# Performance work log

Hardware: AMD Instinct MI355X
Metric: run time of the kernel (lower is better)

## Reference

```python
import jax, jax.numpy as jnp
import numpy as np

N = 16384      # nodes
E = 131072     # edges
D = 768        # in_size = hid_size = out_size (LayerNorm(768) hardcoded)
NT = 4         # num edge types (TypedLinear num_types)
NB = 3         # num bases (basis regularizer)
LN_EPS = 1e-5


def _layernorm(x, gamma, beta):
    mu = jnp.mean(x, axis=-1, keepdims=True)
    var = jnp.mean(jnp.square(x - mu), axis=-1, keepdims=True)
    return (x - mu) * jax.lax.rsqrt(var + LN_EPS) * gamma + beta


def setup_inputs() -> dict:
    key = jax.random.key(0)
    ks = jax.random.split(key, 16)
    s = 0.02  # weight init scale
    return {
        "h": jax.random.normal(ks[0], (N, D), jnp.float32),
        # TypedLinear basis params: W = sum_b coeff[t,b] * basis[b]
        "W_text": jax.random.normal(ks[1], (NB, D, D), jnp.float32) * s,
        "coeff_text": jax.random.normal(ks[2], (NT, NB), jnp.float32),
        "W_user": jax.random.normal(ks[3], (NB, D, D), jnp.float32) * s,
        "coeff_user": jax.random.normal(ks[4], (NT, NB), jnp.float32),
        "W_dst": jax.random.normal(ks[5], (NB, D, D), jnp.float32) * s,
        "coeff_dst": jax.random.normal(ks[6], (NT, NB), jnp.float32),
        "ln_gamma": jnp.ones((D,), jnp.float32),
        "ln_beta": jnp.zeros((D,), jnp.float32),
        "W_lin": jax.random.normal(ks[7], (2 * D, D), jnp.float32) * s,
        "b_lin": jnp.zeros((D,), jnp.float32),
        "src": jax.random.randint(ks[8], (E,), 0, N, dtype=jnp.int32),
        "dst": jax.random.randint(ks[9], (E,), 0, N, dtype=jnp.int32),
        "etype": jax.random.randint(ks[10], (E,), 0, NT, dtype=jnp.int32),
        "hete": jax.random.randint(ks[11], (E,), 0, 2, dtype=jnp.int32),
    }


def reference(h, W_text, coeff_text, W_user, coeff_user, W_dst, coeff_dst,
              ln_gamma, ln_beta, W_lin, b_lin, src, dst, etype, hete):
    # eval mode: dropout = identity
    x = _layernorm(h, ln_gamma, ln_beta)                       # [N, D]
    # Typed-linear via basis decomposition, folded per (type, node): [NT, N, D]
    Ht = jnp.einsum('nd,bdh,tb->tnh', x, W_text, coeff_text)
    Hu = jnp.einsum('nd,bdh,tb->tnh', x, W_user, coeff_user)
    Hd = jnp.einsum('nd,bdh,tb->tnh', x, W_dst, coeff_dst)

    mask = hete > 0                                            # hete vs homo edges
    # per-edge routed source message: [E, D]
    ef = jnp.where(mask[:, None],
                   jax.nn.relu(Ht[etype, src]),
                   jax.nn.relu(Hu[etype, src]))
    # Original concatenates [hete_feat, homo_feat] along edge dim, i.e. a stable
    # permutation putting hete edges first; dst features stay in original order.
    perm = jnp.argsort((~mask).astype(jnp.int32), stable=True)
    feat_perm = ef[perm]                                       # [E, D]
    dfeat = jax.nn.relu(Hd[etype, dst])                        # [E, D]
    m = jnp.concatenate([feat_perm, dfeat], axis=-1)           # [E, 2D]
    # scatter-sum messages to destination nodes
    n = jax.ops.segment_sum(m, dst, num_segments=N)            # [N, 2D]
    z = jax.nn.relu(n @ W_lin + b_lin)                         # [N, D]
    zn = jnp.linalg.norm(z, ord=2, axis=1, keepdims=True)
    zn = jnp.where(zn == 0, jnp.asarray(1.0, z.dtype), zn)
    return z / zn
```

## Files before the change

### kernel.cpp

```cpp
#include <hip/hip_runtime.h>
#include <hip/hip_bf16.h>
#include <cstdint>

static constexpr int N_  = 16384;
static constexpr int E_  = 131072;
static constexpr int D_  = 768;
static constexpr int D2_ = 1536;
static constexpr int DSQ_ = D_ * D_;

static constexpr size_t OFF_XB   = 0;
static constexpr size_t OFF_WBT  = 25165824;
static constexpr size_t OFF_WLT  = 39321600;
static constexpr size_t OFF_NB16 = 41680896;
static constexpr size_t OFF_Y3   = 92012544;
static constexpr size_t OFF_ZB   = 92012544;
static constexpr size_t OFF_N1C  = 192675840;
static constexpr size_t OFF_PAY  = 217841664;
static constexpr size_t OFF_CNT  = 218365952;
static constexpr size_t OFF_CURH = 218628096;
static constexpr size_t OFF_CURU = 218693632;
static constexpr size_t OFF_BASE = 218759168;
static constexpr size_t OFF_BC   = 218824736;
static constexpr size_t OFF_SCAN = 218826784;

typedef __attribute__((ext_vector_type(8))) short short8v;
typedef __attribute__((ext_vector_type(4))) float floatx4;

__device__ __forceinline__ void gld16(const void* g, void* l) {
  __builtin_amdgcn_global_load_lds(
      (const __attribute__((address_space(1))) unsigned int*)g,
      (__attribute__((address_space(3))) unsigned int*)l, 16, 0, 0);
}

__device__ __forceinline__ float b2f(short u) {
  union { unsigned int i; float f; } x;
  x.i = ((unsigned int)(unsigned short)u) << 16;
  return x.f;
}

__device__ __forceinline__ float wave_sum(float v) {
#pragma unroll
  for (int o = 32; o; o >>= 1) v += __shfl_down(v, o, 64);
  return v;
}

__global__ __launch_bounds__(256) void wbasis_t_kernel(
    const float* __restrict__ Wt, const float* __restrict__ Wu,
    const float* __restrict__ Wd, __hip_bfloat16* __restrict__ WbT) {
  __shared__ float tile[64][65];
  int fb = blockIdx.y;
  int f = fb / 3, b = fb % 3;
  const float* W = ((f == 0) ? Wt : ((f == 1) ? Wu : Wd)) + (size_t)b * DSQ_;
  int dt = (blockIdx.x / 12) * 64;
  int ht = (blockIdx.x % 12) * 64;
  int tid = threadIdx.x;
#pragma unroll
  for (int jj = 0; jj < 16; jj++) {
    int idx = jj * 256 + tid;
    int rr = idx >> 6, cc = idx & 63;
    tile[rr][cc] = W[(size_t)(dt + rr) * D_ + ht + cc];
  }
  __syncthreads();
#pragma unroll
  for (int jj = 0; jj < 16; jj++) {
    int idx = jj * 256 + tid;
    int hh = idx >> 6, dd = idx & 63;
    WbT[(size_t)fb * DSQ_ + (size_t)(ht + hh) * D_ + dt + dd] =
        __float2bfloat16(tile[dd][hh]);
  }
}

__global__ __launch_bounds__(256) void wlint_kernel(
    const float* __restrict__ W, __hip_bfloat16* __restrict__ WT) {
  int i = blockIdx.x * 256 + threadIdx.x;
  int k = i / D_, h = i % D_;
  WT[(size_t)h * D2_ + k] = __float2bfloat16(W[i]);
}

__global__ __launch_bounds__(256) void ln_kernel(
    const float* __restrict__ h, const float* __restrict__ gamma,
    const float* __restrict__ beta, __hip_bfloat16* __restrict__ x) {
  int v = blockIdx.x, tid = threadIdx.x;
  const float* hr = h + (size_t)v * D_;
  float e0 = hr[tid], e1 = hr[tid + 256], e2 = hr[tid + 512];
  float s = e0 + e1 + e2;
  float q = e0 * e0 + e1 * e1 + e2 * e2;
  __shared__ float red[8];
  __shared__ float mv[2];
  float ws_ = wave_sum(s), wq = wave_sum(q);
  int lane = tid & 63, w = tid >> 6;
  if (lane == 0) { red[w] = ws_; red[4 + w] = wq; }
  __syncthreads();
  if (tid == 0) {
    float S = red[0] + red[1] + red[2] + red[3];
    float Q = red[4] + red[5] + red[6] + red[7];
    float mu = S * (1.0f / D_);
    float var = Q * (1.0f / D_) - mu * mu;
    mv[0] = mu;
    mv[1] = rsqrtf(var + 1e-5f);
  }
  __syncthreads();
  float mu = mv[0], rstd = mv[1];
  __hip_bfloat16* xr = x + (size_t)v * D_;
  xr[tid]       = __float2bfloat16((e0 - mu) * rstd * gamma[tid]       + beta[tid]);
  xr[tid + 256] = __float2bfloat16((e1 - mu) * rstd * gamma[tid + 256] + beta[tid + 256]);
  xr[tid + 512] = __float2bfloat16((e2 - mu) * rstd * gamma[tid + 512] + beta[tid + 512]);
}

__global__ __launch_bounds__(256) void edge_a_kernel(
    const int* __restrict__ hete, const int* __restrict__ dst,
    const int* __restrict__ etype, int* __restrict__ blockcnt,
    int* __restrict__ cnt4) {
  int j = blockIdx.x * 256 + threadIdx.x;
  int flag = hete[j] > 0;
  unsigned long long m = __ballot(flag);
  __shared__ int wsum[4];
  int lane = threadIdx.x & 63, w = threadIdx.x >> 6;
  if (lane == 0) wsum[w] = __popcll(m);
  __syncthreads();
  if (threadIdx.x == 0)
    blockcnt[blockIdx.x] = wsum[0] + wsum[1] + wsum[2] + wsum[3];
  atomicAdd(&cnt4[dst[j] * 4 + etype[j]], 1);
}

__global__ __launch_bounds__(1024) void fused_scan_kernel(
    const int* __restrict__ blockcnt, int* __restrict__ scanout,
    const int* __restrict__ cnt4, int* __restrict__ base) {
  int t = threadIdx.x;
  if (blockIdx.x == 0) {
    __shared__ int s[1024];
    int v = (t < 512) ? blockcnt[t] : 0;
    s[t] = v;
    __syncthreads();
    for (int o = 1; o < 512; o <<= 1) {
      int add = (t >= o) ? s[t - o] : 0;
      __syncthreads();
      s[t] += add;
      __syncthreads();
    }
    if (t < 512) scanout[t] = s[t] - v;
    if (t == 511) scanout[512] = s[511];
  } else {
    __shared__ int s[1024];
    int loc[16];
    int sum = 0;
#pragma unroll
    for (int i = 0; i < 16; i++) {
      int v = t * 16 + i;
      int d = cnt4[v * 4] + cnt4[v * 4 + 1] + cnt4[v * 4 + 2] + cnt4[v * 4 + 3];
      loc[i] = sum;
      sum += d;
    }
    s[t] = sum;
    __syncthreads();
    for (int o = 1; o < 1024; o <<= 1) {
      int add = (t >= o) ? s[t - o] : 0;
      __syncthreads();
      s[t] += add;
      __syncthreads();
    }
    int pre = t ? s[t - 1] : 0;
#pragma unroll
    for (int i = 0; i < 16; i++) base[t * 16 + i] = pre + loc[i];
    if (t == 1023) base[N_] = s[1023];
  }
}

__global__ __launch_bounds__(256) void edge_bsort_kernel(
    const int* __restrict__ hete, const int* __restrict__ dst,
    const int* __restrict__ src, const int* __restrict__ etype,
    const int* __restrict__ scanout, const int* __restrict__ base,
    int* __restrict__ curH, int* __restrict__ curU,
    int* __restrict__ payload) {
  int j = blockIdx.x * 256 + threadIdx.x;
  int flag = hete[j] > 0;
  unsigned long long m = __ballot(flag);
  __shared__ int wsum[4];
  int lane = threadIdx.x & 63, w = threadIdx.x >> 6;
  if (lane == 0) wsum[w] = __popcll(m);
  __syncthreads();
  int wpre = 0;
#pragma unroll
  for (int i = 0; i < 4; i++) wpre += (i < w) ? wsum[i] : 0;
  int lpre = __popcll(m & ((1ull << lane) - 1ull));
  int hcum = scanout[blockIdx.x] + wpre + lpre;
  int K = scanout[512];
  int e = flag ? hcum : (K + j - hcum);
  int v = dst[e];
  int p;
  if (flag) p = base[v] + atomicAdd(&curH[v], 1);
  else      p = base[v + 1] - 1 - atomicAdd(&curU[v], 1);
  payload[p] = (etype[j] << 14) | src[j];
}

template <bool FIRST, int SEG>
__global__ __launch_bounds__(256) void gather_n1_kernel(
    const __hip_bfloat16* __restrict__ Y, const float* __restrict__ coeff,
    const int* __restrict__ base, const int* __restrict__ hcnt,
    const int* __restrict__ payload, __hip_bfloat16* __restrict__ n1c,
    __hip_bfloat16* __restrict__ nb16) {
  int wv = threadIdx.x >> 6, lane = threadIdx.x & 63;
  int v = blockIdx.x * 4 + wv;
  int bh = base[v] + hcnt[v];
  int lo = (SEG == 0) ? base[v] : bh;
  int hi = (SEG == 0) ? bh : base[v + 1];
  float cf[12];
#pragma unroll
  for (int i = 0; i < 12; i++) cf[i] = coeff[i];
  float acc[12];
  if (FIRST) {
#pragma unroll
    for (int i = 0; i < 12; i++) acc[i] = 0.f;
  } else {
    short8v a8 = *(const short8v*)(n1c + (size_t)v * D_ + lane * 8);
    short4  b4 = *(const short4*)(n1c + (size_t)v * D_ + 512 + lane * 4);
#pragma unroll
    for (int i = 0; i < 8; i++) acc[i] = b2f(a8[i]);
    acc[8] = b2f(b4.x); acc[9] = b2f(b4.y);
    acc[10] = b2f(b4.z); acc[11] = b2f(b4.w);
  }
  const size_t YS = (size_t)N_ * D_;
  for (int idx = lo; idx < hi; ++idx) {
    int pl = payload[idx];
    int t = pl >> 14;
    float c0 = cf[t * 3], c1 = cf[t * 3 + 1], c2 = cf[t * 3 + 2];
    const __hip_bfloat16* r0 = Y + (size_t)(pl & 16383) * D_;
    short8v a0 = *(const short8v*)(r0 + lane * 8);
    short8v a1 = *(const short8v*)(r0 + YS + lane * 8);
    short8v a2 = *(const short8v*)(r0 + 2 * YS + lane * 8);
    short4  b0v = *(const short4*)(r0 + 512 + lane * 4);
    short4  b1v = *(const short4*)(r0 + YS + 512 + lane * 4);
    short4  b2v = *(const short4*)(r0 + 2 * YS + 512 + lane * 4);
#pragma unroll
    for (int i = 0; i < 8; i++)
      acc[i] += fmaxf(c0 * b2f(a0[i]) + c1 * b2f(a1[i]) + c2 * b2f(a2[i]), 0.f);
    acc[8]  += fmaxf(c0 * b2f(b0v.x) + c1 * b2f(b1v.x) + c2 * b2f(b2v.x), 0.f);
    acc[9]  += fmaxf(c0 * b2f(b0v.y) + c1 * b2f(b1v.y) + c2 * b2f(b2v.y), 0.f);
    acc[10] += fmaxf(c0 * b2f(b0v.z) + c1 * b2f(b1v.z) + c2 * b2f(b2v.z), 0.f);
    acc[11] += fmaxf(c0 * b2f(b0v.w) + c1 * b2f(b1v.w) + c2 * b2f(b2v.w), 0.f);
  }
  __hip_bfloat16 o[12];
#pragma unroll
  for (int i = 0; i < 12; i++) o[i] = __float2bfloat16(acc[i]);
  if (FIRST) {
    *(short8v*)(n1c + (size_t)v * D_ + lane * 8) = *(const short8v*)o;
    *(short4*)(n1c + (size_t)v * D_ + 512 + lane * 4) = *(const short4*)(o + 8);
  } else {
    *(short8v*)(nb16 + (size_t)v * D2_ + lane * 8) = *(const short8v*)o;
    *(short4*)(nb16 + (size_t)v * D2_ + 512 + lane * 4) = *(const short4*)(o + 8);
  }
}

__global__ __launch_bounds__(256) void combine_n2_kernel(
    const __hip_bfloat16* __restrict__ Y, const float* __restrict__ cd,
    const int* __restrict__ cnt4, __hip_bfloat16* __restrict__ nb16) {
  size_t i = ((size_t)blockIdx.x * 256 + threadIdx.x) * 8;
  int v = (int)(i / D_);
  int k = (int)(i % D_);
  const size_t YS = (size_t)N_ * D_;
  short8v y0 = *(const short8v*)(Y + i);
  short8v y1 = *(const short8v*)(Y + YS + i);
  short8v y2 = *(const short8v*)(Y + 2 * YS + i);
  float f0[8], f1[8], f2[8];
#pragma unroll
  for (int j = 0; j < 8; j++) {
    f0[j] = b2f(y0[j]); f1[j] = b2f(y1[j]); f2[j] = b2f(y2[j]);
  }
  float acc[8] = {0.f, 0.f, 0.f, 0.f, 0.f, 0.f, 0.f, 0.f};
#pragma unroll
  for (int t = 0; t < 4; t++) {
    float c = (float)cnt4[v * 4 + t];
    if (c != 0.f) {
      float d0 = cd[t * 3], d1 = cd[t * 3 + 1], d2 = cd[t * 3 + 2];
#pragma unroll
      for (int j = 0; j < 8; j++)
        acc[j] += c * fmaxf(d0 * f0[j] + d1 * f1[j] + d2 * f2[j], 0.f);
    }
  }
  __hip_bfloat16 o[8];
#pragma unroll
  for (int j = 0; j < 8; j++) o[j] = __float2bfloat16(acc[j]);
  *(short8v*)(nb16 + (size_t)v * D2_ + D_ + k) = *(const short8v*)o;
}

template <bool BIAS, bool RELU>
__global__ __launch_bounds__(256) void gemm_mfma_kernel(
    const __hip_bfloat16* __restrict__ A, const __hip_bfloat16* __restrict__ BT0,
    const float* __restrict__ bias, __hip_bfloat16* __restrict__ C0,
    int M, int N, int K, size_t strideB, size_t strideC) {
  __shared__ char lds[32768];
  char* As = lds;
  char* Bs = lds + 16384;
  int tid = threadIdx.x;
  int lane = tid & 63;
  int wv = tid >> 6;
  int wr = wv >> 1, wc = wv & 1;
  int gx = gridDim.x, gz = gridDim.z;
  int nwg = gx * gridDim.y * gz;
  int id = (blockIdx.z * gridDim.y + blockIdx.y) * gx + blockIdx.x;
  int s = (id & 7) * (nwg >> 3) + (id >> 3);
  int bx = s % gx;
  int rem = s / gx;
  int z = rem % gz;
  int by = rem / gz;
  const __hip_bfloat16* BT = BT0 + (size_t)z * strideB;
  int row0 = by * 128, col0 = bx * 128;
  int r_ = tid >> 3;
  int s_ = tid & 7;

  floatx4 acc[4][4];
#pragma unroll
  for (int i = 0; i < 4; i++)
#pragma unroll
    for (int j = 0; j < 4; j++) acc[i][j] = floatx4{0.f, 0.f, 0.f, 0.f};

  for (int k0 = 0; k0 < K; k0 += 64) {
    __syncthreads();
#pragma unroll
    for (int is = 0; is < 4; is++) {
      int r = is * 32 + r_;
      int sp = s_ ^ (r & 7);
      gld16(A  + (size_t)(row0 + r) * K + k0 + sp * 8, As + is * 4096 + tid * 16);
      gld16(BT + (size_t)(col0 + r) * K + k0 + sp * 8, Bs + is * 4096 + tid * 16);
    }
    __syncthreads();
#pragma unroll
    for (int kk = 0; kk < 64; kk += 32) {
      int p = (kk >> 3) + (lane >> 4);
      short8v af[4], bf[4];
#pragma unroll
      for (int m = 0; m < 4; m++) {
        int ra = wr * 64 + m * 16 + (lane & 15);
        af[m] = *(const short8v*)(As + ra * 128 + ((p ^ (ra & 7)) << 4));
        int rb = wc * 64 + m * 16 + (lane & 15);
        bf[m] = *(const short8v*)(Bs + rb * 128 + ((p ^ (rb & 7)) << 4));
      }
#pragma unroll
      for (int m = 0; m < 4; m++)
#pragma unroll
        for (int n = 0; n < 4; n++)
          acc[m][n] = __builtin_amdgcn_mfma_f32_16x16x32_bf16(
              af[m], bf[n], acc[m][n], 0, 0, 0);
    }
  }
  __syncthreads();
  char* cs = lds + wv * 8192;
#pragma unroll
  for (int m = 0; m < 4; m++) {
#pragma unroll
    for (int n = 0; n < 4; n++) {
      int c = n * 16 + (lane & 15);
      float bv = BIAS ? bias[col0 + wc * 64 + c] : 0.f;
#pragma unroll
      for (int q = 0; q < 4; q++) {
        int r = m * 16 + (lane >> 4) * 4 + q;
        float v = acc[m][n][q] + bv;
        if (RELU) v = fmaxf(v, 0.f);
        int byte = r * 128 + ((((c >> 3) + r) & 7) << 4) + ((c & 7) << 1);
        *(__hip_bfloat16*)(cs + byte) = __float2bfloat16(v);
      }
    }
  }
  __hip_bfloat16* C = C0 + (size_t)z * strideC;
#pragma unroll
  for (int i = 0; i < 8; i++) {
    int r = i * 8 + (lane >> 3);
    int s8 = lane & 7;
    int p = (s8 + r) & 7;
    short8v v = *(const short8v*)(cs + r * 128 + (p << 4));
    int grow = row0 + wr * 64 + r;
    int gcol = col0 + wc * 64 + s8 * 8;
    *(short8v*)(C + (size_t)grow * N + gcol) = v;
  }
}

__global__ __launch_bounds__(256) void norm_kernel(
    const __hip_bfloat16* __restrict__ z, float* __restrict__ out) {
  int v = blockIdx.x, tid = threadIdx.x;
  float e[4] = {0.f, 0.f, 0.f, 0.f};
  if (tid < 192) {
    short4 a = *(const short4*)(z + (size_t)v * D_ + tid * 4);
    e[0] = b2f(a.x); e[1] = b2f(a.y); e[2] = b2f(a.z); e[3] = b2f(a.w);
  }
  float q = e[0] * e[0] + e[1] * e[1] + e[2] * e[2] + e[3] * e[3];
  __shared__ float red[4];
  __shared__ float sc;
  float wq = wave_sum(q);
  int lane = tid & 63, w = tid >> 6;
  if (lane == 0) red[w] = wq;
  __syncthreads();
  if (tid == 0) {
    float S = red[0] + red[1] + red[2] + red[3];
    float norm = sqrtf(S);
    sc = (norm == 0.f) ? 1.f : (1.f / norm);
  }
  __syncthreads();
  if (tid < 192) {
    float s = sc;
    float4 o = {e[0] * s, e[1] * s, e[2] * s, e[3] * s};
    *(float4*)(out + (size_t)v * D_ + tid * 4) = o;
  }
}

extern "C" void kernel_launch(void* const* d_in, const int* in_sizes, int n_in,
                              void* d_out, int out_size, void* d_ws,
                              size_t ws_size, hipStream_t stream) {
  (void)in_sizes; (void)n_in; (void)out_size; (void)ws_size;
  const float* h      = (const float*)d_in[0];
  const float* W_text = (const float*)d_in[1];
  const float* c_text = (const float*)d_in[2];
  const float* W_user = (const float*)d_in[3];
  const float* c_user = (const float*)d_in[4];
  const float* W_dst  = (const float*)d_in[5];
  const float* c_dst  = (const float*)d_in[6];
  const float* gamma  = (const float*)d_in[7];
  const float* beta   = (const float*)d_in[8];
  const float* W_lin  = (const float*)d_in[9];
  const float* b_lin  = (const float*)d_in[10];
  const int* src      = (const int*)d_in[11];
  const int* dst      = (const int*)d_in[12];
  const int* etype    = (const int*)d_in[13];
  const int* hete     = (const int*)d_in[14];
  float* out          = (float*)d_out;

  char* ws = (char*)d_ws;
  __hip_bfloat16* xb   = (__hip_bfloat16*)(ws + OFF_XB);
  __hip_bfloat16* WbT  = (__hip_bfloat16*)(ws + OFF_WBT);
  __hip_bfloat16* WlT  = (__hip_bfloat16*)(ws + OFF_WLT);
  __hip_bfloat16* nb16 = (__hip_bfloat16*)(ws + OFF_NB16);
  __hip_bfloat16* Y3   = (__hip_bfloat16*)(ws + OFF_Y3);
  __hip_bfloat16* zbuf = (__hip_bfloat16*)(ws + OFF_ZB);
  __hip_bfloat16* n1c  = (__hip_bfloat16*)(ws + OFF_N1C);
  int* payload  = (int*)(ws + OFF_PAY);
  int* cnt4     = (int*)(ws + OFF_CNT);
  int* curH     = (int*)(ws + OFF_CURH);
  int* curU     = (int*)(ws + OFF_CURU);
  int* base     = (int*)(ws + OFF_BASE);
  int* blockcnt = (int*)(ws + OFF_BC);
  int* scanout  = (int*)(ws + OFF_SCAN);

  hipMemsetAsync(cnt4, 0, 262144 + 65536 + 65536, stream);

  wbasis_t_kernel<<<dim3(144, 9), 256, 0, stream>>>(W_text, W_user, W_dst, WbT);
  wlint_kernel<<<(D2_ * D_) / 256, 256, 0, stream>>>(W_lin, WlT);
  ln_kernel<<<N_, 256, 0, stream>>>(h, gamma, beta, xb);
  edge_a_kernel<<<E_ / 256, 256, 0, stream>>>(hete, dst, etype, blockcnt, cnt4);
  fused_scan_kernel<<<2, 1024, 0, stream>>>(blockcnt, scanout, cnt4, base);
  edge_bsort_kernel<<<E_ / 256, 256, 0, stream>>>(hete, dst, src, etype,
                                                  scanout, base, curH, curU,
                                                  payload);

  const size_t HSTRIDE = (size_t)N_ * D_;
  const dim3 ggrid(D_ / 128, N_ / 128, 3);

  gemm_mfma_kernel<false, false><<<ggrid, 256, 0, stream>>>(
      xb, WbT + (size_t)6 * DSQ_, nullptr, Y3, N_, D_, D_, DSQ_, HSTRIDE);
  combine_n2_kernel<<<(N_ * D_) / (256 * 8), 256, 0, stream>>>(Y3, c_dst,
                                                               cnt4, nb16);
  gemm_mfma_kernel<false, false><<<ggrid, 256, 0, stream>>>(
      xb, WbT, nullptr, Y3, N_, D_, D_, DSQ_, HSTRIDE);
  gather_n1_kernel<true, 0><<<N_ / 4, 256, 0, stream>>>(
      Y3, c_text, base, curH, payload, n1c, nb16);
  gemm_mfma_kernel<false, false><<<ggrid, 256, 0, stream>>>(
      xb, WbT + (size_t)3 * DSQ_, nullptr, Y3, N_, D_, D_, DSQ_, HSTRIDE);
  gather_n1_kernel<false, 1><<<N_ / 4, 256, 0, stream>>>(
      Y3, c_user, base, curH, payload, n1c, nb16);

  gemm_mfma_kernel<true, true><<<dim3(D_ / 128, N_ / 128, 1), 256, 0, stream>>>(
      nb16, WlT, b_lin, zbuf, N_, D_, D2_, 0, 0);
  norm_kernel<<<N_, 256, 0, stream>>>(zbuf, out);
}
```

Baseline: 470.3 us.

## Merge text/user GEMMs and gathers into one pass when workspace allows

When the workspace is large enough, the text and user basis GEMMs run as a single 6-slice launch into one big Y buffer. A single merged gather kernel then reads both halves per destination node, instead of two gathers that round-trip an n1c intermediate. The weight transpose kernels are merged into one tiled launch, and the layernorm kernel is vectorized with float4 loads. This trades a larger workspace footprint for fewer launches and less intermediate traffic, and falls back to the old path when the workspace is small.

```diff
diff --git a/kernel.cpp b/kernel.cpp
--- a/kernel.cpp
+++ b/kernel.cpp
@@ -8,20 +8,34 @@
 static constexpr int D2_ = 1536;
 static constexpr int DSQ_ = D_ * D_;
 
-static constexpr size_t OFF_XB   = 0;
-static constexpr size_t OFF_WBT  = 25165824;
-static constexpr size_t OFF_WLT  = 39321600;
-static constexpr size_t OFF_NB16 = 41680896;
-static constexpr size_t OFF_Y3   = 92012544;
-static constexpr size_t OFF_ZB   = 92012544;
-static constexpr size_t OFF_N1C  = 192675840;
-static constexpr size_t OFF_PAY  = 217841664;
-static constexpr size_t OFF_CNT  = 218365952;
-static constexpr size_t OFF_CURH = 218628096;
-static constexpr size_t OFF_CURU = 218693632;
-static constexpr size_t OFF_BASE = 218759168;
-static constexpr size_t OFF_BC   = 218824736;
-static constexpr size_t OFF_SCAN = 218826784;
+static constexpr size_t S_XB   = 0;
+static constexpr size_t S_WBT  = 25165824;
+static constexpr size_t S_WLT  = 39321600;
+static constexpr size_t S_NB16 = 41680896;
+static constexpr size_t S_Y3   = 92012544;
+static constexpr size_t S_ZB   = 92012544;
+static constexpr size_t S_N1C  = 192675840;
+static constexpr size_t S_PAY  = 217841664;
+static constexpr size_t S_CNT  = 218365952;
+static constexpr size_t S_CURH = 218628096;
+static constexpr size_t S_CURU = 218693632;
+static constexpr size_t S_BASE = 218759168;
+static constexpr size_t S_BC   = 218824736;
+static constexpr size_t S_SCAN = 218826784;
+
+static constexpr size_t B_XB   = 0;
+static constexpr size_t B_WBT  = 25165824;
+static constexpr size_t B_WLT  = 35782656;
+static constexpr size_t B_NB16 = 38141952;
+static constexpr size_t B_PAY  = 88473600;
+static constexpr size_t B_CNT  = 88997888;
+static constexpr size_t B_CURH = 89260032;
+static constexpr size_t B_CURU = 89325568;
+static constexpr size_t B_BASE = 89391104;
+static constexpr size_t B_BC   = 89456672;
+static constexpr size_t B_SCAN = 89458720;
+static constexpr size_t B_YBIG = 89460992;
+static constexpr size_t B_NEED = 240455936;
 
 typedef __attribute__((ext_vector_type(8))) short short8v;
 typedef __attribute__((ext_vector_type(4))) float floatx4;
@@ -44,47 +58,68 @@
   return v;
 }
 
-__global__ __launch_bounds__(256) void wbasis_t_kernel(
+__global__ __launch_bounds__(256) void wprep_kernel(
     const float* __restrict__ Wt, const float* __restrict__ Wu,
-    const float* __restrict__ Wd, __hip_bfloat16* __restrict__ WbT) {
+    const float* __restrict__ Wd, const float* __restrict__ Wl,
+    __hip_bfloat16* __restrict__ WbT, __hip_bfloat16* __restrict__ WlT) {
   __shared__ float tile[64][65];
-  int fb = blockIdx.y;
-  int f = fb / 3, b = fb % 3;
-  const float* W = ((f == 0) ? Wt : ((f == 1) ? Wu : Wd)) + (size_t)b * DSQ_;
-  int dt = (blockIdx.x / 12) * 64;
-  int ht = (blockIdx.x % 12) * 64;
+  int y = blockIdx.y;
   int tid = threadIdx.x;
-#pragma unroll
-  for (int jj = 0; jj < 16; jj++) {
-    int idx = jj * 256 + tid;
-    int rr = idx >> 6, cc = idx & 63;
-    tile[rr][cc] = W[(size_t)(dt + rr) * D_ + ht + cc];
-  }
-  __syncthreads();
-#pragma unroll
-  for (int jj = 0; jj < 16; jj++) {
-    int idx = jj * 256 + tid;
-    int hh = idx >> 6, dd = idx & 63;
-    WbT[(size_t)fb * DSQ_ + (size_t)(ht + hh) * D_ + dt + dd] =
-        __float2bfloat16(tile[dd][hh]);
-  }
-}
-
-__global__ __launch_bounds__(256) void wlint_kernel(
-    const float* __restrict__ W, __hip_bfloat16* __restrict__ WT) {
-  int i = blockIdx.x * 256 + threadIdx.x;
-  int k = i / D_, h = i % D_;
-  WT[(size_t)h * D2_ + k] = __float2bfloat16(W[i]);
+  if (y < 9) {
+    int f = y / 3, b = y % 3;
+    const float* W = ((f == 0) ? Wt : ((f == 1) ? Wu : Wd)) + (size_t)b * DSQ_;
+    int dt = (blockIdx.x / 12) * 64;
+    int ht = (blockIdx.x % 12) * 64;
+#pragma unroll
+    for (int jj = 0; jj < 16; jj++) {
+      int idx = jj * 256 + tid;
+      int rr = idx >> 6, cc = idx & 63;
+      tile[rr][cc] = W[(size_t)(dt + rr) * D_ + ht + cc];
+    }
+    __syncthreads();
+#pragma unroll
+    for (int jj = 0; jj < 16; jj++) {
+      int idx = jj * 256 + tid;
+      int hh = idx >> 6, dd = idx & 63;
+      WbT[(size_t)y * DSQ_ + (size_t)(ht + hh) * D_ + dt + dd] =
+          __float2bfloat16(tile[dd][hh]);
+    }
+  } else {
+    int idx0 = (y - 9) * 144 + blockIdx.x;
+    int kt = (idx0 % 24) * 64;
+    int ht = (idx0 / 24) * 64;
+#pragma unroll
+    for (int jj = 0; jj < 16; jj++) {
+      int idx = jj * 256 + tid;
+      int rr = idx >> 6, cc = idx & 63;
+      tile[rr][cc] = Wl[(size_t)(kt + rr) * D_ + ht + cc];
+    }
+    __syncthreads();
+#pragma unroll
+    for (int jj = 0; jj < 16; jj++) {
+      int idx = jj * 256 + tid;
+      int hh = idx >> 6, dd = idx & 63;
+      WlT[(size_t)(ht + hh) * D2_ + kt + dd] = __float2bfloat16(tile[dd][hh]);
+    }
+  }
 }
 
 __global__ __launch_bounds__(256) void ln_kernel(
     const float* __restrict__ h, const float* __restrict__ gamma,
     const float* __restrict__ beta, __hip_bfloat16* __restrict__ x) {
   int v = blockIdx.x, tid = threadIdx.x;
-  const float* hr = h + (size_t)v * D_;
-  float e0 = hr[tid], e1 = hr[tid + 256], e2 = hr[tid + 512];
-  float s = e0 + e1 + e2;
-  float q = e0 * e0 + e1 * e1 + e2 * e2;
+  float e[4] = {0.f, 0.f, 0.f, 0.f};
+  float g[4], bta[4];
+  if (tid < 192) {
+    float4 a = *(const float4*)(h + (size_t)v * D_ + tid * 4);
+    e[0] = a.x; e[1] = a.y; e[2] = a.z; e[3] = a.w;
+    float4 gg = *(const float4*)(gamma + tid * 4);
+    float4 bb = *(const float4*)(beta + tid * 4);
+    g[0] = gg.x; g[1] = gg.y; g[2] = gg.z; g[3] = gg.w;
+    bta[0] = bb.x; bta[1] = bb.y; bta[2] = bb.z; bta[3] = bb.w;
+  }
+  float s = e[0] + e[1] + e[2] + e[3];
+  float q = e[0] * e[0] + e[1] * e[1] + e[2] * e[2] + e[3] * e[3];
   __shared__ float red[8];
   __shared__ float mv[2];
   float ws_ = wave_sum(s), wq = wave_sum(q);
@@ -100,11 +135,14 @@
     mv[1] = rsqrtf(var + 1e-5f);
   }
   __syncthreads();
-  float mu = mv[0], rstd = mv[1];
-  __hip_bfloat16* xr = x + (size_t)v * D_;
-  xr[tid]       = __float2bfloat16((e0 - mu) * rstd * gamma[tid]       + beta[tid]);
-  xr[tid + 256] = __float2bfloat16((e1 - mu) * rstd * gamma[tid + 256] + beta[tid + 256]);
-  xr[tid + 512] = __float2bfloat16((e2 - mu) * rstd * gamma[tid + 512] + beta[tid + 512]);
+  if (tid < 192) {
+    float mu = mv[0], rstd = mv[1];
+    __hip_bfloat16 o[4];
+#pragma unroll
+    for (int i = 0; i < 4; i++)
+      o[i] = __float2bfloat16((e[i] - mu) * rstd * g[i] + bta[i]);
+    *(short4*)(x + (size_t)v * D_ + tid * 4) = *(const short4*)o;
+  }
 }
 
 __global__ __launch_bounds__(256) void edge_a_kernel(
@@ -249,6 +287,52 @@
     *(short8v*)(nb16 + (size_t)v * D2_ + lane * 8) = *(const short8v*)o;
     *(short4*)(nb16 + (size_t)v * D2_ + 512 + lane * 4) = *(const short4*)(o + 8);
   }
+}
+
+__global__ __launch_bounds__(256) void gather_merged_kernel(
+    const __hip_bfloat16* __restrict__ Yt, const __hip_bfloat16* __restrict__ Yu,
+    const float* __restrict__ c_text, const float* __restrict__ c_user,
+    const int* __restrict__ base, const int* __restrict__ hcnt,
+    const int* __restrict__ payload, __hip_bfloat16* __restrict__ nb16) {
+  int wv = threadIdx.x >> 6, lane = threadIdx.x & 63;
+  int v = blockIdx.x * 4 + wv;
+  int lo = base[v];
+  int bh = lo + hcnt[v];
+  int hi = base[v + 1];
+  float cf[24];
+#pragma unroll
+  for (int i = 0; i < 12; i++) { cf[i] = c_text[i]; cf[12 + i] = c_user[i]; }
+  float acc[12];
+#pragma unroll
+  for (int i = 0; i < 12; i++) acc[i] = 0.f;
+  const size_t YS = (size_t)N_ * D_;
+  for (int idx = lo; idx < hi; ++idx) {
+    int pl = payload[idx];
+    bool isU = idx >= bh;
+    const __hip_bfloat16* Y = isU ? Yu : Yt;
+    int t = pl >> 14;
+    const float* c = cf + (isU ? 12 : 0) + t * 3;
+    float c0 = c[0], c1 = c[1], c2 = c[2];
+    const __hip_bfloat16* r0 = Y + (size_t)(pl & 16383) * D_;
+    short8v a0 = *(const short8v*)(r0 + lane * 8);
+    short8v a1 = *(const short8v*)(r0 + YS + lane * 8);
+    short8v a2 = *(const short8v*)(r0 + 2 * YS + lane * 8);
+    short4  b0v = *(const short4*)(r0 + 512 + lane * 4);
+    short4  b1v = *(const short4*)(r0 + YS + 512 + lane * 4);
+    short4  b2v = *(const short4*)(r0 + 2 * YS + 512 + lane * 4);
+#pragma unroll
+    for (int i = 0; i < 8; i++)
+      acc[i] += fmaxf(c0 * b2f(a0[i]) + c1 * b2f(a1[i]) + c2 * b2f(a2[i]), 0.f);
+    acc[8]  += fmaxf(c0 * b2f(b0v.x) + c1 * b2f(b1v.x) + c2 * b2f(b2v.x), 0.f);
+    acc[9]  += fmaxf(c0 * b2f(b0v.y) + c1 * b2f(b1v.y) + c2 * b2f(b2v.y), 0.f);
+    acc[10] += fmaxf(c0 * b2f(b0v.z) + c1 * b2f(b1v.z) + c2 * b2f(b2v.z), 0.f);
+    acc[11] += fmaxf(c0 * b2f(b0v.w) + c1 * b2f(b1v.w) + c2 * b2f(b2v.w), 0.f);
+  }
+  __hip_bfloat16 o[12];
+#pragma unroll
+  for (int i = 0; i < 12; i++) o[i] = __float2bfloat16(acc[i]);
+  *(short8v*)(nb16 + (size_t)v * D2_ + lane * 8) = *(const short8v*)o;
+  *(short4*)(nb16 + (size_t)v * D2_ + 512 + lane * 4) = *(const short4*)(o + 8);
 }
 
 __global__ __launch_bounds__(256) void combine_n2_kernel(
@@ -405,7 +489,7 @@
 extern "C" void kernel_launch(void* const* d_in, const int* in_sizes, int n_in,
                               void* d_out, int out_size, void* d_ws,
                               size_t ws_size, hipStream_t stream) {
-  (void)in_sizes; (void)n_in; (void)out_size; (void)ws_size;
+  (void)in_sizes; (void)n_in; (void)out_size;
   const float* h      = (const float*)d_in[0];
   const float* W_text = (const float*)d_in[1];
   const float* c_text = (const float*)d_in[2];
@@ -423,26 +507,25 @@
   const int* hete     = (const int*)d_in[14];
   float* out          = (float*)d_out;
 
+  const bool big = ws_size >= (size_t)B_NEED;
   char* ws = (char*)d_ws;
-  __hip_bfloat16* xb   = (__hip_bfloat16*)(ws + OFF_XB);
-  __hip_bfloat16* WbT  = (__hip_bfloat16*)(ws + OFF_WBT);
-  __hip_bfloat16* WlT  = (__hip_bfloat16*)(ws + OFF_WLT);
-  __hip_bfloat16* nb16 = (__hip_bfloat16*)(ws + OFF_NB16);
-  __hip_bfloat16* Y3   = (__hip_bfloat16*)(ws + OFF_Y3);
-  __hip_bfloat16* zbuf = (__hip_bfloat16*)(ws + OFF_ZB);
-  __hip_bfloat16* n1c  = (__hip_bfloat16*)(ws + OFF_N1C);
-  int* payload  = (int*)(ws + OFF_PAY);
-  int* cnt4     = (int*)(ws + OFF_CNT);
-  int* curH     = (int*)(ws + OFF_CURH);
-  int* curU     = (int*)(ws + OFF_CURU);
-  int* base     = (int*)(ws + OFF_BASE);
-  int* blockcnt = (int*)(ws + OFF_BC);
-  int* scanout  = (int*)(ws + OFF_SCAN);
+  const size_t HSTRIDE = (size_t)N_ * D_;
+
+  __hip_bfloat16* xb   = (__hip_bfloat16*)(ws + (big ? B_XB : S_XB));
+  __hip_bfloat16* WbT  = (__hip_bfloat16*)(ws + (big ? B_WBT : S_WBT));
+  __hip_bfloat16* WlT  = (__hip_bfloat16*)(ws + (big ? B_WLT : S_WLT));
+  __hip_bfloat16* nb16 = (__hip_bfloat16*)(ws + (big ? B_NB16 : S_NB16));
+  int* payload  = (int*)(ws + (big ? B_PAY : S_PAY));
+  int* cnt4     = (int*)(ws + (big ? B_CNT : S_CNT));
+  int* curH     = (int*)(ws + (big ? B_CURH : S_CURH));
+  int* curU     = (int*)(ws + (big ? B_CURU : S_CURU));
+  int* base     = (int*)(ws + (big ? B_BASE : S_BASE));
+  int* blockcnt = (int*)(ws + (big ? B_BC : S_BC));
+  int* scanout  = (int*)(ws + (big ? B_SCAN : S_SCAN));
 
   hipMemsetAsync(cnt4, 0, 262144 + 65536 + 65536, stream);
-
-  wbasis_t_kernel<<<dim3(144, 9), 256, 0, stream>>>(W_text, W_user, W_dst, WbT);
-  wlint_kernel<<<(D2_ * D_) / 256, 256, 0, stream>>>(W_lin, WlT);
+  wprep_kernel<<<dim3(144, 11), 256, 0, stream>>>(W_text, W_user, W_dst,
+                                                  W_lin, WbT, WlT);
   ln_kernel<<<N_, 256, 0, stream>>>(h, gamma, beta, xb);
   edge_a_kernel<<<E_ / 256, 256, 0, stream>>>(hete, dst, etype, blockcnt, cnt4);
   fused_scan_kernel<<<2, 1024, 0, stream>>>(blockcnt, scanout, cnt4, base);
@@ -450,23 +533,48 @@
                                                   scanout, base, curH, curU,
                                                   payload);
 
-  const size_t HSTRIDE = (size_t)N_ * D_;
-  const dim3 ggrid(D_ / 128, N_ / 128, 3);
-
-  gemm_mfma_kernel<false, false><<<ggrid, 256, 0, stream>>>(
-      xb, WbT + (size_t)6 * DSQ_, nullptr, Y3, N_, D_, D_, DSQ_, HSTRIDE);
-  combine_n2_kernel<<<(N_ * D_) / (256 * 8), 256, 0, stream>>>(Y3, c_dst,
-                                                               cnt4, nb16);
-  gemm_mfma_kernel<false, false><<<ggrid, 256, 0, stream>>>(
-      xb, WbT, nullptr, Y3, N_, D_, D_, DSQ_, HSTRIDE);
-  gather_n1_kernel<true, 0><<<N_ / 4, 256, 0, stream>>>(
-      Y3, c_text, base, curH, payload, n1c, nb16);
-  gemm_mfma_kernel<false, false><<<ggrid, 256, 0, stream>>>(
-      xb, WbT + (size_t)3 * DSQ_, nullptr, Y3, N_, D_, D_, DSQ_, HSTRIDE);
-  gather_n1_kernel<false, 1><<<N_ / 4, 256, 0, stream>>>(
-      Y3, c_user, base, curH, payload, n1c, nb16);
-
-  gemm_mfma_kernel<true, true><<<dim3(D_ / 128, N_ / 128, 1), 256, 0, stream>>>(
-      nb16, WlT, b_lin, zbuf, N_, D_, D2_, 0, 0);
-  norm_kernel<<<N_, 256, 0, stream>>>(zbuf, out);
-}
+  if (big) {
+    __hip_bfloat16* Ybig = (__hip_bfloat16*)(ws + B_YBIG);
+    __hip_bfloat16* zbuf = Ybig;
+    gemm_mfma_kernel<false, false>
+        <<<dim3(D_ / 128, N_ / 128, 3), 256, 0, stream>>>(
+            xb, WbT + (size_t)6 * DSQ_, nullptr, Ybig, N_, D_, D_, DSQ_,
+            HSTRIDE);
+    combine_n2_kernel<<<(N_ * D_) / (256 * 8), 256, 0, stream>>>(Ybig, c_dst,
+                                                                 cnt4, nb16);
+    gemm_mfma_kernel<false, false>
+        <<<dim3(D_ / 128, N_ / 128, 6), 256, 0, stream>>>(
+            xb, WbT, nullptr, Ybig, N_, D_, D_, DSQ_, HSTRIDE);
+    gather_merged_kernel<<<N_ / 4, 256, 0, stream>>>(
+        Ybig, Ybig + 3 * HSTRIDE, c_text, c_user, base, curH, payload, nb16);
+    gemm_mfma_kernel<true, true>
+        <<<dim3(D_ / 128, N_ / 128, 1), 256, 0, stream>>>(
+            nb16, WlT, b_lin, zbuf, N_, D_, D2_, 0, 0);
+    norm_kernel<<<N_, 256, 0, stream>>>(zbuf, out);
+  } else {
+    __hip_bfloat16* Y3   = (__hip_bfloat16*)(ws + S_Y3);
+    __hip_bfloat16* zbuf = (__hip_bfloat16*)(ws + S_ZB);
+    __hip_bfloat16* n1c  = (__hip_bfloat16*)(ws + S_N1C);
+    gemm_mfma_kernel<false, false>
+        <<<dim3(D_ / 128, N_ / 128, 3), 256, 0, stream>>>(
+            xb, WbT + (size_t)6 * DSQ_, nullptr, Y3, N_, D_, D_, DSQ_,
+            HSTRIDE);
+    combine_n2_kernel<<<(N_ * D_) / (256 * 8), 256, 0, stream>>>(Y3, c_dst,
+                                                                 cnt4, nb16);
+    gemm_mfma_kernel<false, false>
+        <<<dim3(D_ / 128, N_ / 128, 3), 256, 0, stream>>>(
+            xb, WbT, nullptr, Y3, N_, D_, D_, DSQ_, HSTRIDE);
+    gather_n1_kernel<true, 0><<<N_ / 4, 256, 0, stream>>>(
+        Y3, c_text, base, curH, payload, n1c, nb16);
+    gemm_mfma_kernel<false, false>
+        <<<dim3(D_ / 128, N_ / 128, 3), 256, 0, stream>>>(
+            xb, WbT + (size_t)3 * DSQ_, nullptr, Y3, N_, D_, D_, DSQ_,
+            HSTRIDE);
+    gather_n1_kernel<false, 1><<<N_ / 4, 256, 0, stream>>>(
+        Y3, c_user, base, curH, payload, n1c, nb16);
+    gemm_mfma_kernel<true, true>
+        <<<dim3(D_ / 128, N_ / 128, 1), 256, 0, stream>>>(
+            nb16, WlT, b_lin, zbuf, N_, D_, D2_, 0, 0);
+    norm_kernel<<<N_, 256, 0, stream>>>(zbuf, out);
+  }
+}
```

Result: slower. 496.5 us (+5.6%).

## Interleave per-basis GEMM outputs per node and merge weight prep kernels

Applied to the files above, without the earlier changes.

The three per-basis projection outputs are now stored interleaved per node (row stride 3*D) instead of as three separate N×D planes. Each gathered source row's three basis vectors then sit contiguously, which should improve locality for the random-row gathers and the combine kernel. The W_lin transpose is folded into the tiled basis-transpose kernel using an LDS tile, replacing a strided uncoalesced transpose. LayerNorm is vectorized to float4 loads and short4 stores.

```diff
diff --git a/kernel.cpp b/kernel.cpp
--- a/kernel.cpp
+++ b/kernel.cpp
@@ -6,6 +6,7 @@
 static constexpr int E_  = 131072;
 static constexpr int D_  = 768;
 static constexpr int D2_ = 1536;
+static constexpr int D3_ = 2304;
 static constexpr int DSQ_ = D_ * D_;
 
 static constexpr size_t OFF_XB   = 0;
@@ -44,47 +45,68 @@
   return v;
 }
 
-__global__ __launch_bounds__(256) void wbasis_t_kernel(
+__global__ __launch_bounds__(256) void wprep_kernel(
     const float* __restrict__ Wt, const float* __restrict__ Wu,
-    const float* __restrict__ Wd, __hip_bfloat16* __restrict__ WbT) {
+    const float* __restrict__ Wd, const float* __restrict__ Wl,
+    __hip_bfloat16* __restrict__ WbT, __hip_bfloat16* __restrict__ WlT) {
   __shared__ float tile[64][65];
-  int fb = blockIdx.y;
-  int f = fb / 3, b = fb % 3;
-  const float* W = ((f == 0) ? Wt : ((f == 1) ? Wu : Wd)) + (size_t)b * DSQ_;
-  int dt = (blockIdx.x / 12) * 64;
-  int ht = (blockIdx.x % 12) * 64;
+  int y = blockIdx.y;
   int tid = threadIdx.x;
-#pragma unroll
-  for (int jj = 0; jj < 16; jj++) {
-    int idx = jj * 256 + tid;
-    int rr = idx >> 6, cc = idx & 63;
-    tile[rr][cc] = W[(size_t)(dt + rr) * D_ + ht + cc];
-  }
-  __syncthreads();
-#pragma unroll
-  for (int jj = 0; jj < 16; jj++) {
-    int idx = jj * 256 + tid;
-    int hh = idx >> 6, dd = idx & 63;
-    WbT[(size_t)fb * DSQ_ + (size_t)(ht + hh) * D_ + dt + dd] =
-        __float2bfloat16(tile[dd][hh]);
-  }
-}
-
-__global__ __launch_bounds__(256) void wlint_kernel(
-    const float* __restrict__ W, __hip_bfloat16* __restrict__ WT) {
-  int i = blockIdx.x * 256 + threadIdx.x;
-  int k = i / D_, h = i % D_;
-  WT[(size_t)h * D2_ + k] = __float2bfloat16(W[i]);
+  if (y < 9) {
+    int f = y / 3, b = y % 3;
+    const float* W = ((f == 0) ? Wt : ((f == 1) ? Wu : Wd)) + (size_t)b * DSQ_;
+    int dt = (blockIdx.x / 12) * 64;
+    int ht = (blockIdx.x % 12) * 64;
+#pragma unroll
+    for (int jj = 0; jj < 16; jj++) {
+      int idx = jj * 256 + tid;
+      int rr = idx >> 6, cc = idx & 63;
+      tile[rr][cc] = W[(size_t)(dt + rr) * D_ + ht + cc];
+    }
+    __syncthreads();
+#pragma unroll
+    for (int jj = 0; jj < 16; jj++) {
+      int idx = jj * 256 + tid;
+      int hh = idx >> 6, dd = idx & 63;
+      WbT[(size_t)y * DSQ_ + (size_t)(ht + hh) * D_ + dt + dd] =
+          __float2bfloat16(tile[dd][hh]);
+    }
+  } else {
+    int idx0 = (y - 9) * 144 + blockIdx.x;
+    int kt = (idx0 % 24) * 64;
+    int ht = (idx0 / 24) * 64;
+#pragma unroll
+    for (int jj = 0; jj < 16; jj++) {
+      int idx = jj * 256 + tid;
+      int rr = idx >> 6, cc = idx & 63;
+      tile[rr][cc] = Wl[(size_t)(kt + rr) * D_ + ht + cc];
+    }
+    __syncthreads();
+#pragma unroll
+    for (int jj = 0; jj < 16; jj++) {
+      int idx = jj * 256 + tid;
+      int hh = idx >> 6, dd = idx & 63;
+      WlT[(size_t)(ht + hh) * D2_ + kt + dd] = __float2bfloat16(tile[dd][hh]);
+    }
+  }
 }
 
 __global__ __launch_bounds__(256) void ln_kernel(
     const float* __restrict__ h, const float* __restrict__ gamma,
     const float* __restrict__ beta, __hip_bfloat16* __restrict__ x) {
   int v = blockIdx.x, tid = threadIdx.x;
-  const float* hr = h + (size_t)v * D_;
-  float e0 = hr[tid], e1 = hr[tid + 256], e2 = hr[tid + 512];
-  float s = e0 + e1 + e2;
-  float q = e0 * e0 + e1 * e1 + e2 * e2;
+  float e[4] = {0.f, 0.f, 0.f, 0.f};
+  float g[4], bta[4];
+  if (tid < 192) {
+    float4 a = *(const float4*)(h + (size_t)v * D_ + tid * 4);
+    e[0] = a.x; e[1] = a.y; e[2] = a.z; e[3] = a.w;
+    float4 gg = *(const float4*)(gamma + tid * 4);
+    float4 bb = *(const float4*)(beta + tid * 4);
+    g[0] = gg.x; g[1] = gg.y; g[2] = gg.z; g[3] = gg.w;
+    bta[0] = bb.x; bta[1] = bb.y; bta[2] = bb.z; bta[3] = bb.w;
+  }
+  float s = e[0] + e[1] + e[2] + e[3];
+  float q = e[0] * e[0] + e[1] * e[1] + e[2] * e[2] + e[3] * e[3];
   __shared__ float red[8];
   __shared__ float mv[2];
   float ws_ = wave_sum(s), wq = wave_sum(q);
@@ -100,11 +122,14 @@
     mv[1] = rsqrtf(var + 1e-5f);
   }
   __syncthreads();
-  float mu = mv[0], rstd = mv[1];
-  __hip_bfloat16* xr = x + (size_t)v * D_;
-  xr[tid]       = __float2bfloat16((e0 - mu) * rstd * gamma[tid]       + beta[tid]);
-  xr[tid + 256] = __float2bfloat16((e1 - mu) * rstd * gamma[tid + 256] + beta[tid + 256]);
-  xr[tid + 512] = __float2bfloat16((e2 - mu) * rstd * gamma[tid + 512] + beta[tid + 512]);
+  if (tid < 192) {
+    float mu = mv[0], rstd = mv[1];
+    __hip_bfloat16 o[4];
+#pragma unroll
+    for (int i = 0; i < 4; i++)
+      o[i] = __float2bfloat16((e[i] - mu) * rstd * g[i] + bta[i]);
+    *(short4*)(x + (size_t)v * D_ + tid * 4) = *(const short4*)o;
+  }
 }
 
 __global__ __launch_bounds__(256) void edge_a_kernel(
@@ -219,18 +244,17 @@
     acc[8] = b2f(b4.x); acc[9] = b2f(b4.y);
     acc[10] = b2f(b4.z); acc[11] = b2f(b4.w);
   }
-  const size_t YS = (size_t)N_ * D_;
   for (int idx = lo; idx < hi; ++idx) {
     int pl = payload[idx];
     int t = pl >> 14;
     float c0 = cf[t * 3], c1 = cf[t * 3 + 1], c2 = cf[t * 3 + 2];
-    const __hip_bfloat16* r0 = Y + (size_t)(pl & 16383) * D_;
+    const __hip_bfloat16* r0 = Y + (size_t)(pl & 16383) * D3_;
     short8v a0 = *(const short8v*)(r0 + lane * 8);
-    short8v a1 = *(const short8v*)(r0 + YS + lane * 8);
-    short8v a2 = *(const short8v*)(r0 + 2 * YS + lane * 8);
+    short8v a1 = *(const short8v*)(r0 + D_ + lane * 8);
+    short8v a2 = *(const short8v*)(r0 + 2 * D_ + lane * 8);
     short4  b0v = *(const short4*)(r0 + 512 + lane * 4);
-    short4  b1v = *(const short4*)(r0 + YS + 512 + lane * 4);
-    short4  b2v = *(const short4*)(r0 + 2 * YS + 512 + lane * 4);
+    short4  b1v = *(const short4*)(r0 + D_ + 512 + lane * 4);
+    short4  b2v = *(const short4*)(r0 + 2 * D_ + 512 + lane * 4);
 #pragma unroll
     for (int i = 0; i < 8; i++)
       acc[i] += fmaxf(c0 * b2f(a0[i]) + c1 * b2f(a1[i]) + c2 * b2f(a2[i]), 0.f);
@@ -257,10 +281,10 @@
   size_t i = ((size_t)blockIdx.x * 256 + threadIdx.x) * 8;
   int v = (int)(i / D_);
   int k = (int)(i % D_);
-  const size_t YS = (size_t)N_ * D_;
-  short8v y0 = *(const short8v*)(Y + i);
-  short8v y1 = *(const short8v*)(Y + YS + i);
-  short8v y2 = *(const short8v*)(Y + 2 * YS + i);
+  const __hip_bfloat16* yr = Y + (size_t)v * D3_ + k;
+  short8v y0 = *(const short8v*)(yr);
+  short8v y1 = *(const short8v*)(yr + D_);
+  short8v y2 = *(const short8v*)(yr + 2 * D_);
   float f0[8], f1[8], f2[8];
 #pragma unroll
   for (int j = 0; j < 8; j++) {
@@ -287,7 +311,7 @@
 __global__ __launch_bounds__(256) void gemm_mfma_kernel(
     const __hip_bfloat16* __restrict__ A, const __hip_bfloat16* __restrict__ BT0,
     const float* __restrict__ bias, __hip_bfloat16* __restrict__ C0,
-    int M, int N, int K, size_t strideB, size_t strideC) {
+    int M, int N, int K, size_t strideB, int ldC, int zcol) {
   __shared__ char lds[32768];
   char* As = lds;
   char* Bs = lds + 16384;
@@ -361,7 +385,7 @@
       }
     }
   }
-  __hip_bfloat16* C = C0 + (size_t)z * strideC;
+  __hip_bfloat16* C = C0 + (size_t)z * zcol;
 #pragma unroll
   for (int i = 0; i < 8; i++) {
     int r = i * 8 + (lane >> 3);
@@ -370,7 +394,7 @@
     short8v v = *(const short8v*)(cs + r * 128 + (p << 4));
     int grow = row0 + wr * 64 + r;
     int gcol = col0 + wc * 64 + s8 * 8;
-    *(short8v*)(C + (size_t)grow * N + gcol) = v;
+    *(short8v*)(C + (size_t)grow * ldC + gcol) = v;
   }
 }
 
@@ -441,8 +465,8 @@
 
   hipMemsetAsync(cnt4, 0, 262144 + 65536 + 65536, stream);
 
-  wbasis_t_kernel<<<dim3(144, 9), 256, 0, stream>>>(W_text, W_user, W_dst, WbT);
-  wlint_kernel<<<(D2_ * D_) / 256, 256, 0, stream>>>(W_lin, WlT);
+  wprep_kernel<<<dim3(144, 11), 256, 0, stream>>>(W_text, W_user, W_dst,
+                                                  W_lin, WbT, WlT);
   ln_kernel<<<N_, 256, 0, stream>>>(h, gamma, beta, xb);
   edge_a_kernel<<<E_ / 256, 256, 0, stream>>>(hete, dst, etype, blockcnt, cnt4);
   fused_scan_kernel<<<2, 1024, 0, stream>>>(blockcnt, scanout, cnt4, base);
@@ -450,23 +474,22 @@
                                                   scanout, base, curH, curU,
                                                   payload);
 
-  const size_t HSTRIDE = (size_t)N_ * D_;
   const dim3 ggrid(D_ / 128, N_ / 128, 3);
 
   gemm_mfma_kernel<false, false><<<ggrid, 256, 0, stream>>>(
-      xb, WbT + (size_t)6 * DSQ_, nullptr, Y3, N_, D_, D_, DSQ_, HSTRIDE);
+      xb, WbT + (size_t)6 * DSQ_, nullptr, Y3, N_, D_, D_, DSQ_, D3_, D_);
   combine_n2_kernel<<<(N_ * D_) / (256 * 8), 256, 0, stream>>>(Y3, c_dst,
                                                                cnt4, nb16);
   gemm_mfma_kernel<false, false><<<ggrid, 256, 0, stream>>>(
-      xb, WbT, nullptr, Y3, N_, D_, D_, DSQ_, HSTRIDE);
+      xb, WbT, nullptr, Y3, N_, D_, D_, DSQ_, D3_, D_);
   gather_n1_kernel<true, 0><<<N_ / 4, 256, 0, stream>>>(
       Y3, c_text, base, curH, payload, n1c, nb16);
   gemm_mfma_kernel<false, false><<<ggrid, 256, 0, stream>>>(
-      xb, WbT + (size_t)3 * DSQ_, nullptr, Y3, N_, D_, D_, DSQ_, HSTRIDE);
+      xb, WbT + (size_t)3 * DSQ_, nullptr, Y3, N_, D_, D_, DSQ_, D3_, D_);
   gather_n1_kernel<false, 1><<<N_ / 4, 256, 0, stream>>>(
       Y3, c_user, base, curH, payload, n1c, nb16);
 
   gemm_mfma_kernel<true, true><<<dim3(D_ / 128, N_ / 128, 1), 256, 0, stream>>>(
-      nb16, WlT, b_lin, zbuf, N_, D_, D2_, 0, 0);
+      nb16, WlT, b_lin, zbuf, N_, D_, D2_, 0, D_, 0);
   norm_kernel<<<N_, 256, 0, stream>>>(zbuf, out);
 }
```

Measured after the change: 456.5 us. 1.03x faster.
